# Kernel optimization log

Hardware: AMD Instinct MI355X
Metric: run time of the kernel (lower is better)

Reference implementation:

```python
import jax, jax.numpy as jnp
import numpy as np

B, N, NQ, C = 4, 16384, 1024, 128
NS = 64          # nsample
RADIUS = 0.3     # ball-query fallback radius


def setup_inputs() -> dict:
    key = jax.random.key(0)
    k1, k2, k3, k4 = jax.random.split(key, 4)
    key_xyz = jax.random.uniform(k1, (B, N, 3), dtype=jnp.float32)
    key_features = jax.random.normal(k2, (B, C, N), dtype=jnp.float32)
    centers = jax.random.uniform(k3, (B, NQ, 3), dtype=jnp.float32)
    # box sizes L/H/W in [0.05, 0.25]
    sizes = 0.05 + 0.2 * jax.random.uniform(k4, (B, NQ, 3), dtype=jnp.float32)
    query_xyz = jnp.concatenate([centers, sizes], axis=-1)
    return {"key_xyz": key_xyz, "key_features": key_features, "query_xyz": query_xyz}


def _box_group(key_xyz, key_features, query_xyz):
    centers = query_xyz[:, :, :3]              # [B,nq,3]
    half = 0.5 * query_xyz[:, :, 3:]           # [B,nq,3] half box extents

    # per-query per-key absolute offsets: [B,nq,N,3]
    d = jnp.abs(key_xyz[:, None, :, :] - centers[:, :, None, :])
    inside = jnp.all(d <= half[:, :, None, :], axis=-1)      # [B,nq,N] AABB test
    dist2 = jnp.sum(d * d, axis=-1)                          # [B,nq,N]

    # ball-query fallback for queries whose box contains no point
    has_box = jnp.any(inside, axis=-1)                       # [B,nq]
    sel = jnp.where(has_box[..., None], inside, dist2 <= RADIUS * RADIUS)

    # first NS selected indices (stable sort puts selected points first,
    # preserving ascending key index order -> deterministic box_query semantics)
    order = jnp.argsort((~sel).astype(jnp.int32), axis=-1)[:, :, :NS]  # [B,nq,NS]

    count = jnp.minimum(jnp.sum(sel, axis=-1), NS)           # [B,nq]
    pad = jnp.arange(NS)[None, None, :] >= count[..., None]  # True = padded slot
    idx = jnp.where(pad, 0, order)                           # pad with index 0
    mask = pad.at[:, :, 0].set(False)                        # cuda path: mask[...,0]=False

    # gathers
    g_xyz = jax.vmap(lambda k, i: k[i])(key_xyz, idx)        # [B,nq,NS,3]
    g_xyz = g_xyz - centers[:, :, None, :]                   # recenter on query
    grouped_xyz = jnp.transpose(g_xyz, (0, 3, 1, 2))         # [B,3,nq,NS]
    grouped_feat = jax.vmap(lambda f, i: f[:, i])(key_features, idx)  # [B,C,nq,NS]
    return grouped_xyz, grouped_feat, mask


def reference(key_xyz, key_features, query_xyz):
    return _box_group(key_xyz, key_features, query_xyz)
```

## Files before the change

### kernel.cpp

```cpp
#include <hip/hip_runtime.h>

#pragma clang fp contract(off)

#define B_  4
#define N_  16384
#define NQ_ 1024
#define C_  128
#define NS_ 64
#define G_  16
#define NCELL_ 4096
#define MAXCELLS_ 344
#define SELCAP_ 1024

#define OFF_IDX    ((size_t)0)
#define SZ_IDX     ((size_t)B_*NQ_*NS_*4)
#define OFF_FEAT   ((size_t)(1u<<20))
#define SZ_FEAT    ((size_t)B_*N_*C_*4)
#define OFF_COUNTS (OFF_FEAT + SZ_FEAT)
#define OFF_CSTART (OFF_COUNTS + (size_t)B_*NCELL_*4)
#define OFF_CURSOR (OFF_CSTART + (size_t)B_*NCELL_*4)
#define OFF_PLIST  (OFF_CURSOR + (size_t)B_*NCELL_*4)
#define WS_NEED    (OFF_PLIST + (size_t)B_*N_*4)

__global__ __launch_bounds__(256) void zero_k(int* __restrict__ counts) {
    int id = blockIdx.x * 256 + threadIdx.x;
    if (id < B_ * NCELL_) counts[id] = 0;
}

__device__ __forceinline__ int cell_of(float x, float y, float z) {
    int ix = (int)(x * (float)G_); ix = min(G_ - 1, max(0, ix));
    int iy = (int)(y * (float)G_); iy = min(G_ - 1, max(0, iy));
    int iz = (int)(z * (float)G_); iz = min(G_ - 1, max(0, iz));
    return ix + (iy << 4) + (iz << 8);
}

__global__ __launch_bounds__(256) void bin_count_k(const float* __restrict__ key_xyz,
                                                   int* __restrict__ counts) {
    int id = blockIdx.x * 256 + threadIdx.x;
    int b = id >> 14, n = id & (N_ - 1);
    const float* p = key_xyz + ((size_t)b * N_ + n) * 3;
    int cid = cell_of(p[0], p[1], p[2]);
    atomicAdd(&counts[(b << 12) + cid], 1);
}

__global__ __launch_bounds__(1024) void scan_k(const int* __restrict__ counts,
                                               int* __restrict__ cstart,
                                               int* __restrict__ cursor) {
    __shared__ int a[1024];
    int b = blockIdx.x, t = threadIdx.x;
    int base = b << 12;
    int c0 = t * 4;
    int v0 = counts[base + c0 + 0], v1 = counts[base + c0 + 1];
    int v2 = counts[base + c0 + 2], v3 = counts[base + c0 + 3];
    int s = v0 + v1 + v2 + v3;
    a[t] = s;
    __syncthreads();
    for (int o = 1; o < 1024; o <<= 1) {
        int add = (t >= o) ? a[t - o] : 0;
        __syncthreads();
        a[t] += add;
        __syncthreads();
    }
    int excl = a[t] - s;
    int e0 = excl, e1 = e0 + v0, e2 = e1 + v1, e3 = e2 + v2;
    cstart[base + c0 + 0] = e0; cursor[base + c0 + 0] = e0;
    cstart[base + c0 + 1] = e1; cursor[base + c0 + 1] = e1;
    cstart[base + c0 + 2] = e2; cursor[base + c0 + 2] = e2;
    cstart[base + c0 + 3] = e3; cursor[base + c0 + 3] = e3;
}

__global__ __launch_bounds__(256) void scatter_k(const float* __restrict__ key_xyz,
                                                 int* __restrict__ cursor,
                                                 int* __restrict__ plist) {
    int id = blockIdx.x * 256 + threadIdx.x;
    int b = id >> 14, n = id & (N_ - 1);
    const float* p = key_xyz + ((size_t)b * N_ + n) * 3;
    int cid = cell_of(p[0], p[1], p[2]);
    int pos = atomicAdd(&cursor[(b << 12) + cid], 1);
    plist[(b << 14) + pos] = n;
}

__global__ __launch_bounds__(256) void fused_ts_k(
    const float* __restrict__ key_xyz, const float* __restrict__ key_feat,
    const float* __restrict__ query,
    const int* __restrict__ counts, const int* __restrict__ cstart,
    const int* __restrict__ plist,
    float* __restrict__ feat_t, int* __restrict__ idx_out,
    float* __restrict__ out_xyz, float* __restrict__ out_mask)
{
    __shared__ float ttile[32][33];
    __shared__ int s_ccnt[MAXCELLS_];
    __shared__ int s_cstart[MAXCELLS_];
    __shared__ int s_pref[MAXCELLS_ + 1];
    __shared__ int s_sel[SELCAP_];
    __shared__ int s_scnt;
    __shared__ int s_list[4][NS_];
    __shared__ int s_cnt4[4];

    int t = threadIdx.x;

    if (blockIdx.x >= B_ * NQ_) {
        int id2 = blockIdx.x - B_ * NQ_;
        int n0 = (id2 & 511) * 32;
        int c0 = ((id2 >> 9) & 3) * 32;
        int b  = id2 >> 11;
        int x = t & 31, y = t >> 5;
#pragma unroll
        for (int k = 0; k < 4; ++k)
            ttile[y + 8*k][x] = key_feat[((size_t)b * C_ + c0 + y + 8*k) * N_ + n0 + x];
        __syncthreads();
#pragma unroll
        for (int k = 0; k < 4; ++k)
            feat_t[((size_t)b * N_ + n0 + y + 8*k) * C_ + c0 + x] = ttile[x][y + 8*k];
        return;
    }

    int bq = blockIdx.x;
    int b  = bq >> 10;
    int q  = bq & (NQ_ - 1);
    int wave = t >> 6, lane = t & 63;

    const float* qp = query + (size_t)bq * 6;
    float cx = qp[0], cy = qp[1], cz = qp[2];
    float hx = 0.5f * qp[3], hy = 0.5f * qp[4], hz = 0.5f * qp[5];
    const float* kb = key_xyz + (size_t)b * N_ * 3;

    if (t == 0) s_scnt = 0;

    int ilox = max(0, (int)floorf((cx - hx) * (float)G_) - 1);
    int ihix = min(G_ - 1, (int)floorf((cx + hx) * (float)G_) + 1);
    int iloy = max(0, (int)floorf((cy - hy) * (float)G_) - 1);
    int ihiy = min(G_ - 1, (int)floorf((cy + hy) * (float)G_) + 1);
    int iloz = max(0, (int)floorf((cz - hz) * (float)G_) - 1);
    int ihiz = min(G_ - 1, (int)floorf((cz + hz) * (float)G_) + 1);
    int nx = ihix - ilox + 1, ny = ihiy - iloy + 1, nz = ihiz - iloz + 1;
    int ncells = nx * ny * nz;

    for (int ci = t; ci < ncells; ci += 256) {
        int iz = ci / (nx * ny);
        int r  = ci - iz * (nx * ny);
        int iy = r / nx;
        int ix = r - iy * nx;
        int cid = (ilox + ix) + ((iloy + iy) << 4) + ((iloz + iz) << 8);
        s_ccnt[ci]   = counts[(b << 12) + cid];
        s_cstart[ci] = cstart[(b << 12) + cid];
    }
    __syncthreads();

    if (wave == 0) {
        int run = 0;
        for (int base = 0; base < ncells; base += 64) {
            int x = (base + lane < ncells) ? s_ccnt[base + lane] : 0;
            int own = x;
#pragma unroll
            for (int o = 1; o < 64; o <<= 1) {
                int v = __shfl_up(x, (unsigned)o);
                if (lane >= o) x += v;
            }
            if (base + lane < ncells) s_pref[base + lane] = run + x - own;
            run += __shfl(x, 63);
        }
        if (lane == 0) s_pref[ncells] = run;
    }
    __syncthreads();

    int total = s_pref[ncells];
    for (int i = t; i < total; i += 256) {
        int lo = 0, hi = ncells;
        while (hi - lo > 1) {
            int mid = (lo + hi) >> 1;
            if (s_pref[mid] <= i) lo = mid; else hi = mid;
        }
        int n = plist[(b << 14) + s_cstart[lo] + (i - s_pref[lo])];
        float dx = fabsf(kb[3*n + 0] - cx);
        float dy = fabsf(kb[3*n + 1] - cy);
        float dz = fabsf(kb[3*n + 2] - cz);
        if (dx <= hx && dy <= hy && dz <= hz) {
            int pos = atomicAdd(&s_scnt, 1);
            if (pos < SELCAP_) s_sel[pos] = n;
        }
    }
    __syncthreads();
    int scnt = s_scnt;

    if (scnt > 0) {
        int m = 64;
        while (m < scnt && m < SELCAP_) m <<= 1;
        for (int i = t; i < m; i += 256)
            if (i >= scnt) s_sel[i] = 0x7fffffff;
        __syncthreads();
        for (int k = 2; k <= m; k <<= 1) {
            for (int j = k >> 1; j > 0; j >>= 1) {
                for (int i = t; i < m; i += 256) {
                    int ixj = i ^ j;
                    if (ixj > i) {
                        int va = s_sel[i], vb = s_sel[ixj];
                        bool up = ((i & k) == 0);
                        if ((va > vb) == up) { s_sel[i] = vb; s_sel[ixj] = va; }
                    }
                }
                __syncthreads();
            }
        }
        int count = min(scnt, NS_);
        if (t < NS_) {
            int j = t;
            int idx = (j < count) ? s_sel[j] : 0;
            idx_out[(size_t)bq * NS_ + j] = idx;
            out_mask[(size_t)bq * NS_ + j] = (j >= count && j > 0) ? 1.0f : 0.0f;
            float px = kb[3*idx + 0] - cx;
            float py = kb[3*idx + 1] - cy;
            float pz = kb[3*idx + 2] - cz;
            size_t xb = ((size_t)b * 3) * NQ_ * NS_ + (size_t)q * NS_ + j;
            out_xyz[xb]                       = px;
            out_xyz[xb +     (size_t)NQ_*NS_] = py;
            out_xyz[xb + 2 * (size_t)NQ_*NS_] = pz;
        }
    } else {
        const float R2 = (float)(0.3 * 0.3);
        const int seg = N_ / 4;
        int n0s = wave * seg;
        unsigned long long lt = (1ull << lane) - 1ull;
        int cnt = 0;
        for (int it = 0; it < seg / 64; ++it) {
            int n = n0s + it * 64 + lane;
            float dx = kb[3*n + 0] - cx;
            float dy = kb[3*n + 1] - cy;
            float dz = kb[3*n + 2] - cz;
            float d2 = dx*dx + dy*dy + dz*dz;
            bool r = d2 <= R2;
            unsigned long long mmask = __ballot(r);
            if (r) {
                int p = cnt + __popcll(mmask & lt);
                if (p < NS_) s_list[wave][p] = n;
            }
            cnt += __popcll(mmask);
            if (cnt >= NS_) break;
        }
        if (lane == 0) s_cnt4[wave] = cnt;
        __syncthreads();
        if (wave == 0) {
            int c0s = min(s_cnt4[0], NS_);
            int c1s = min(s_cnt4[1], NS_);
            int c2s = min(s_cnt4[2], NS_);
            int tot   = s_cnt4[0] + s_cnt4[1] + s_cnt4[2] + s_cnt4[3];
            int count = min(tot, NS_);
            int j = lane;
            int idx = 0;
            if (j < count) {
                int o1 = c0s, o2 = o1 + c1s, o3 = o2 + c2s;
                if      (j < o1) idx = s_list[0][j];
                else if (j < o2) idx = s_list[1][j - o1];
                else if (j < o3) idx = s_list[2][j - o2];
                else             idx = s_list[3][j - o3];
            }
            idx_out[(size_t)bq * NS_ + j] = idx;
            out_mask[(size_t)bq * NS_ + j] = (j >= count && j > 0) ? 1.0f : 0.0f;
            float px = kb[3*idx + 0] - cx;
            float py = kb[3*idx + 1] - cy;
            float pz = kb[3*idx + 2] - cz;
            size_t xb = ((size_t)b * 3) * NQ_ * NS_ + (size_t)q * NS_ + j;
            out_xyz[xb]                       = px;
            out_xyz[xb +     (size_t)NQ_*NS_] = py;
            out_xyz[xb + 2 * (size_t)NQ_*NS_] = pz;
        }
    }
}

__global__ __launch_bounds__(256) void select_lin_k(
    const float* __restrict__ key_xyz, const float* __restrict__ query,
    int* __restrict__ idx_out, float* __restrict__ out_xyz,
    float* __restrict__ out_mask)
{
    int bq = blockIdx.x;
    int b  = bq >> 10;
    int q  = bq & (NQ_ - 1);
    int t    = threadIdx.x;
    int wave = t >> 6;
    int lane = t & 63;

    __shared__ int s_list[4][NS_];
    __shared__ int s_cnt[4];

    const float* qp = query + (size_t)bq * 6;
    float cx = qp[0], cy = qp[1], cz = qp[2];
    float hx = 0.5f * qp[3], hy = 0.5f * qp[4], hz = 0.5f * qp[5];
    const float* kb = key_xyz + (size_t)b * N_ * 3;

    const int seg = N_ / 4;
    int n0 = wave * seg;
    unsigned long long lt = (1ull << lane) - 1ull;

    int cnt = 0;
    for (int it = 0; it < seg / 64; ++it) {
        int n = n0 + it * 64 + lane;
        float dx = fabsf(kb[3*n + 0] - cx);
        float dy = fabsf(kb[3*n + 1] - cy);
        float dz = fabsf(kb[3*n + 2] - cz);
        bool inside = (dx <= hx) && (dy <= hy) && (dz <= hz);
        unsigned long long m = __ballot(inside);
        if (inside) {
            int p = cnt + __popcll(m & lt);
            if (p < NS_) s_list[wave][p] = n;
        }
        cnt += __popcll(m);
        if (cnt >= NS_) break;
    }
    if (lane == 0) s_cnt[wave] = cnt;
    __syncthreads();

    int ti = s_cnt[0] + s_cnt[1] + s_cnt[2] + s_cnt[3];
    if (ti == 0) {
        const float R2 = (float)(0.3 * 0.3);
        cnt = 0;
        for (int it = 0; it < seg / 64; ++it) {
            int n = n0 + it * 64 + lane;
            float dx = kb[3*n + 0] - cx;
            float dy = kb[3*n + 1] - cy;
            float dz = kb[3*n + 2] - cz;
            float d2 = dx*dx + dy*dy + dz*dz;
            bool r = d2 <= R2;
            unsigned long long m = __ballot(r);
            if (r) {
                int p = cnt + __popcll(m & lt);
                if (p < NS_) s_list[wave][p] = n;
            }
            cnt += __popcll(m);
            if (cnt >= NS_) break;
        }
        if (lane == 0) s_cnt[wave] = cnt;
    }
    __syncthreads();

    if (wave == 0) {
        int c0s = min(s_cnt[0], NS_);
        int c1s = min(s_cnt[1], NS_);
        int c2s = min(s_cnt[2], NS_);
        int tot   = s_cnt[0] + s_cnt[1] + s_cnt[2] + s_cnt[3];
        int count = min(tot, NS_);
        int j = lane;
        int idx = 0;
        if (j < count) {
            int o1 = c0s, o2 = o1 + c1s, o3 = o2 + c2s;
            if      (j < o1) idx = s_list[0][j];
            else if (j < o2) idx = s_list[1][j - o1];
            else if (j < o3) idx = s_list[2][j - o2];
            else             idx = s_list[3][j - o3];
        }
        idx_out[(size_t)bq * NS_ + j] = idx;
        out_mask[(size_t)bq * NS_ + j] = (j >= count && j > 0) ? 1.0f : 0.0f;
        float px = kb[3*idx + 0] - cx;
        float py = kb[3*idx + 1] - cy;
        float pz = kb[3*idx + 2] - cz;
        size_t xb = ((size_t)b * 3) * NQ_ * NS_ + (size_t)q * NS_ + j;
        out_xyz[xb]                       = px;
        out_xyz[xb +     (size_t)NQ_*NS_] = py;
        out_xyz[xb + 2 * (size_t)NQ_*NS_] = pz;
    }
}

__global__ __launch_bounds__(512) void gather_k(
    const float* __restrict__ feat_t, const int* __restrict__ idx_in,
    const float* __restrict__ key_feat, float* __restrict__ out_feat, int use_t)
{
    int bq = blockIdx.x;
    int b  = bq >> 10;
    int q  = bq & (NQ_ - 1);
    int t    = threadIdx.x;
    int wave = t >> 6;
    int lane = t & 63;

    __shared__ int   s_idx[NS_];
    __shared__ float tile[NS_][129];

    if (t < NS_) s_idx[t] = idx_in[(size_t)bq * NS_ + t];
    __syncthreads();

    float* ob = out_feat + (size_t)b * C_ * NQ_ * NS_ + (size_t)q * NS_;
    if (use_t) {
        const float4* ft4 = (const float4*)feat_t;
#pragma unroll
        for (int k = 0; k < 4; ++k) {
            int u  = t + k * 512;
            int j  = u >> 5;
            int c4 = u & 31;
            float4 v = ft4[((size_t)b * N_ + s_idx[j]) * (C_ / 4) + c4];
            tile[j][c4*4 + 0] = v.x;
            tile[j][c4*4 + 1] = v.y;
            tile[j][c4*4 + 2] = v.z;
            tile[j][c4*4 + 3] = v.w;
        }
        __syncthreads();
#pragma unroll
        for (int c = wave; c < C_; c += 8)
            __builtin_nontemporal_store(tile[lane][c],
                                        &ob[(size_t)c * NQ_ * NS_ + lane]);
    } else {
        const float* fb = key_feat + (size_t)b * C_ * N_;
        int idx = s_idx[lane];
        for (int c = wave; c < C_; c += 8)
            ob[(size_t)c * NQ_ * NS_ + lane] = fb[(size_t)c * N_ + idx];
    }
}

extern "C" void kernel_launch(void* const* d_in, const int* in_sizes, int n_in,
                              void* d_out, int out_size, void* d_ws, size_t ws_size,
                              hipStream_t stream) {
    const float* key_xyz  = (const float*)d_in[0];
    const float* key_feat = (const float*)d_in[1];
    const float* query    = (const float*)d_in[2];

    float* out      = (float*)d_out;
    float* out_xyz  = out;
    float* out_feat = out + (size_t)B_ * 3 * NQ_ * NS_;
    float* out_mask = out_feat + (size_t)B_ * C_ * NQ_ * NS_;

    char* ws = (char*)d_ws;
    int*   d_idx   = (int*)(ws + OFF_IDX);
    float* ft      = (float*)(ws + OFF_FEAT);
    int*   counts  = (int*)(ws + OFF_COUNTS);
    int*   cstartp = (int*)(ws + OFF_CSTART);
    int*   cursor  = (int*)(ws + OFF_CURSOR);
    int*   plist   = (int*)(ws + OFF_PLIST);

    if (ws_size >= WS_NEED) {
        zero_k<<<dim3((B_ * NCELL_ + 255) / 256), dim3(256), 0, stream>>>(counts);
        bin_count_k<<<dim3(B_ * N_ / 256), dim3(256), 0, stream>>>(key_xyz, counts);
        scan_k<<<dim3(B_), dim3(1024), 0, stream>>>(counts, cstartp, cursor);
        scatter_k<<<dim3(B_ * N_ / 256), dim3(256), 0, stream>>>(key_xyz, cursor, plist);
        fused_ts_k<<<dim3(B_ * NQ_ + B_ * (C_ / 32) * (N_ / 32)), dim3(256), 0, stream>>>(
            key_xyz, key_feat, query, counts, cstartp, plist,
            ft, d_idx, out_xyz, out_mask);
        gather_k<<<dim3(B_ * NQ_), dim3(512), 0, stream>>>(
            ft, d_idx, key_feat, out_feat, 1);
    } else {
        select_lin_k<<<dim3(B_ * NQ_), dim3(256), 0, stream>>>(
            key_xyz, query, d_idx, out_xyz, out_mask);
        gather_k<<<dim3(B_ * NQ_), dim3(512), 0, stream>>>(
            ft, d_idx, key_feat, out_feat, 0);
    }
}
```

Before: 216.6 us.

## Fuse selection with feature gather and move transpose into scatter kernel

The box selection and the feature gather are merged into one 512-thread kernel, so the intermediate index buffer round trip and one launch go away. The feature transpose now runs in the scatter kernel, with point lists storing xyz plus index as float4 so the selection reads coordinates without a second indirection. Small selections are sorted with a wave-level shuffle bitonic sort. Block IDs are remapped for XCD locality and the ball fallback is split across 8 waves. In exchange the fused kernel uses more shared memory and registers, which may lower occupancy, and the gather now runs in two channel chunks.

Measured after the change: 211.0 us. 1.03x faster.

```diff
diff --git a/kernel.cpp b/kernel.cpp
--- a/kernel.cpp
+++ b/kernel.cpp
@@ -12,26 +12,24 @@
 #define MAXCELLS_ 344
 #define SELCAP_ 1024
 
-#define OFF_IDX    ((size_t)0)
-#define SZ_IDX     ((size_t)B_*NQ_*NS_*4)
-#define OFF_FEAT   ((size_t)(1u<<20))
+#define OFF_FEAT   ((size_t)0)
 #define SZ_FEAT    ((size_t)B_*N_*C_*4)
 #define OFF_COUNTS (OFF_FEAT + SZ_FEAT)
 #define OFF_CSTART (OFF_COUNTS + (size_t)B_*NCELL_*4)
 #define OFF_CURSOR (OFF_CSTART + (size_t)B_*NCELL_*4)
-#define OFF_PLIST  (OFF_CURSOR + (size_t)B_*NCELL_*4)
-#define WS_NEED    (OFF_PLIST + (size_t)B_*N_*4)
-
-__global__ __launch_bounds__(256) void zero_k(int* __restrict__ counts) {
-    int id = blockIdx.x * 256 + threadIdx.x;
-    if (id < B_ * NCELL_) counts[id] = 0;
-}
+#define OFF_PLIST4 (OFF_CURSOR + (size_t)B_*NCELL_*4)
+#define WS_NEED    (OFF_PLIST4 + (size_t)B_*N_*16)
 
 __device__ __forceinline__ int cell_of(float x, float y, float z) {
     int ix = (int)(x * (float)G_); ix = min(G_ - 1, max(0, ix));
     int iy = (int)(y * (float)G_); iy = min(G_ - 1, max(0, iy));
     int iz = (int)(z * (float)G_); iz = min(G_ - 1, max(0, iz));
     return ix + (iy << 4) + (iz << 8);
+}
+
+__global__ __launch_bounds__(256) void zero_k(int* __restrict__ counts) {
+    int id = blockIdx.x * 256 + threadIdx.x;
+    if (id < B_ * NCELL_) counts[id] = 0;
 }
 
 __global__ __launch_bounds__(256) void bin_count_k(const float* __restrict__ key_xyz,
@@ -69,55 +67,64 @@
     cstart[base + c0 + 3] = e3; cursor[base + c0 + 3] = e3;
 }
 
-__global__ __launch_bounds__(256) void scatter_k(const float* __restrict__ key_xyz,
-                                                 int* __restrict__ cursor,
-                                                 int* __restrict__ plist) {
-    int id = blockIdx.x * 256 + threadIdx.x;
-    int b = id >> 14, n = id & (N_ - 1);
-    const float* p = key_xyz + ((size_t)b * N_ + n) * 3;
-    int cid = cell_of(p[0], p[1], p[2]);
-    int pos = atomicAdd(&cursor[(b << 12) + cid], 1);
-    plist[(b << 14) + pos] = n;
-}
-
-__global__ __launch_bounds__(256) void fused_ts_k(
+#define TBLK_ (B_ * (C_/32) * (N_/32))
+__global__ __launch_bounds__(256) void scatter_transpose_k(
     const float* __restrict__ key_xyz, const float* __restrict__ key_feat,
-    const float* __restrict__ query,
-    const int* __restrict__ counts, const int* __restrict__ cstart,
-    const int* __restrict__ plist,
-    float* __restrict__ feat_t, int* __restrict__ idx_out,
-    float* __restrict__ out_xyz, float* __restrict__ out_mask)
+    int* __restrict__ cursor, float4* __restrict__ plist4,
+    float* __restrict__ feat_t)
 {
     __shared__ float ttile[32][33];
-    __shared__ int s_ccnt[MAXCELLS_];
-    __shared__ int s_cstart[MAXCELLS_];
-    __shared__ int s_pref[MAXCELLS_ + 1];
-    __shared__ int s_sel[SELCAP_];
-    __shared__ int s_scnt;
-    __shared__ int s_list[4][NS_];
-    __shared__ int s_cnt4[4];
-
     int t = threadIdx.x;
-
-    if (blockIdx.x >= B_ * NQ_) {
-        int id2 = blockIdx.x - B_ * NQ_;
-        int n0 = (id2 & 511) * 32;
-        int c0 = ((id2 >> 9) & 3) * 32;
-        int b  = id2 >> 11;
+    if (blockIdx.x < TBLK_) {
+        int id2 = blockIdx.x;
+        int b   = id2 >> 11;
+        int rem = id2 & 2047;
+        int c0  = (rem >> 9) * 32;
+        int n0  = (rem & 511) * 32;
         int x = t & 31, y = t >> 5;
 #pragma unroll
         for (int k = 0; k < 4; ++k)
-            ttile[y + 8*k][x] = key_feat[((size_t)b * C_ + c0 + y + 8*k) * N_ + n0 + x];
+            ttile[y + 8*k][x] = __builtin_nontemporal_load(
+                &key_feat[((size_t)b * C_ + c0 + y + 8*k) * N_ + n0 + x]);
         __syncthreads();
 #pragma unroll
         for (int k = 0; k < 4; ++k)
             feat_t[((size_t)b * N_ + n0 + y + 8*k) * C_ + c0 + x] = ttile[x][y + 8*k];
         return;
     }
-
-    int bq = blockIdx.x;
-    int b  = bq >> 10;
-    int q  = bq & (NQ_ - 1);
+    int id = (blockIdx.x - TBLK_) * 256 + t;
+    int b = id >> 14, n = id & (N_ - 1);
+    const float* p = key_xyz + ((size_t)b * N_ + n) * 3;
+    float x = p[0], y = p[1], z = p[2];
+    int cid = cell_of(x, y, z);
+    int pos = atomicAdd(&cursor[(b << 12) + cid], 1);
+    plist4[(b << 14) + pos] = make_float4(x, y, z, __int_as_float(n));
+}
+
+__global__ __launch_bounds__(512) void selgather_k(
+    const float* __restrict__ key_xyz, const float* __restrict__ query,
+    const int* __restrict__ counts, const int* __restrict__ cstart,
+    const float4* __restrict__ plist4, const float* __restrict__ feat_t,
+    float* __restrict__ out_xyz, float* __restrict__ out_feat,
+    float* __restrict__ out_mask)
+{
+    __shared__ int   s_ccnt[MAXCELLS_];
+    __shared__ int   s_cstart[MAXCELLS_];
+    __shared__ int   s_pref[MAXCELLS_ + 1];
+    __shared__ int   s_sel[SELCAP_];
+    __shared__ int   s_scnt;
+    __shared__ int   s_list[8][NS_];
+    __shared__ int   s_cnt8[8];
+    __shared__ int   s_idx[NS_];
+    __shared__ int   s_count;
+    __shared__ float tile[NS_][65];
+
+    int i    = blockIdx.x;
+    int xcd  = i & 7;
+    int b    = xcd >> 1;
+    int q    = ((i >> 3) << 1) | (xcd & 1);
+    int bq   = (b << 10) | q;
+    int t    = threadIdx.x;
     int wave = t >> 6, lane = t & 63;
 
     const float* qp = query + (size_t)bq * 6;
@@ -136,7 +143,7 @@
     int nx = ihix - ilox + 1, ny = ihiy - iloy + 1, nz = ihiz - iloz + 1;
     int ncells = nx * ny * nz;
 
-    for (int ci = t; ci < ncells; ci += 256) {
+    for (int ci = t; ci < ncells; ci += 512) {
         int iz = ci / (nx * ny);
         int r  = ci - iz * (nx * ny);
         int iy = r / nx;
@@ -165,62 +172,70 @@
     __syncthreads();
 
     int total = s_pref[ncells];
-    for (int i = t; i < total; i += 256) {
+    const float4* pl = plist4 + ((size_t)b << 14);
+    for (int ii = t; ii < total; ii += 512) {
         int lo = 0, hi = ncells;
         while (hi - lo > 1) {
             int mid = (lo + hi) >> 1;
-            if (s_pref[mid] <= i) lo = mid; else hi = mid;
-        }
-        int n = plist[(b << 14) + s_cstart[lo] + (i - s_pref[lo])];
-        float dx = fabsf(kb[3*n + 0] - cx);
-        float dy = fabsf(kb[3*n + 1] - cy);
-        float dz = fabsf(kb[3*n + 2] - cz);
+            if (s_pref[mid] <= ii) lo = mid; else hi = mid;
+        }
+        float4 p = pl[s_cstart[lo] + (ii - s_pref[lo])];
+        float dx = fabsf(p.x - cx);
+        float dy = fabsf(p.y - cy);
+        float dz = fabsf(p.z - cz);
         if (dx <= hx && dy <= hy && dz <= hz) {
             int pos = atomicAdd(&s_scnt, 1);
-            if (pos < SELCAP_) s_sel[pos] = n;
-        }
-    }
-    __syncthreads();
-    int scnt = s_scnt;
+            if (pos < SELCAP_) s_sel[pos] = __float_as_int(p.w);
+        }
+    }
+    __syncthreads();
+    int scnt = min(s_scnt, SELCAP_);
 
     if (scnt > 0) {
-        int m = 64;
-        while (m < scnt && m < SELCAP_) m <<= 1;
-        for (int i = t; i < m; i += 256)
-            if (i >= scnt) s_sel[i] = 0x7fffffff;
-        __syncthreads();
-        for (int k = 2; k <= m; k <<= 1) {
-            for (int j = k >> 1; j > 0; j >>= 1) {
-                for (int i = t; i < m; i += 256) {
-                    int ixj = i ^ j;
-                    if (ixj > i) {
-                        int va = s_sel[i], vb = s_sel[ixj];
-                        bool up = ((i & k) == 0);
-                        if ((va > vb) == up) { s_sel[i] = vb; s_sel[ixj] = va; }
+        int count = min(scnt, NS_);
+        if (scnt <= NS_) {
+            if (wave == 0) {
+                int v = (lane < scnt) ? s_sel[lane] : 0x7fffffff;
+#pragma unroll
+                for (int k = 2; k <= 64; k <<= 1) {
+                    for (int j = k >> 1; j > 0; j >>= 1) {
+                        int pv = __shfl_xor(v, (unsigned)j);
+                        bool dir   = (lane & k) == 0;
+                        bool lower = (lane & j) == 0;
+                        int mn = min(v, pv), mx = max(v, pv);
+                        v = dir ? (lower ? mn : mx) : (lower ? mx : mn);
                     }
                 }
-                __syncthreads();
-            }
-        }
-        int count = min(scnt, NS_);
-        if (t < NS_) {
-            int j = t;
-            int idx = (j < count) ? s_sel[j] : 0;
-            idx_out[(size_t)bq * NS_ + j] = idx;
-            out_mask[(size_t)bq * NS_ + j] = (j >= count && j > 0) ? 1.0f : 0.0f;
-            float px = kb[3*idx + 0] - cx;
-            float py = kb[3*idx + 1] - cy;
-            float pz = kb[3*idx + 2] - cz;
-            size_t xb = ((size_t)b * 3) * NQ_ * NS_ + (size_t)q * NS_ + j;
-            out_xyz[xb]                       = px;
-            out_xyz[xb +     (size_t)NQ_*NS_] = py;
-            out_xyz[xb + 2 * (size_t)NQ_*NS_] = pz;
+                s_idx[lane] = (lane < count) ? v : 0;
+                if (lane == 0) s_count = count;
+            }
+        } else {
+            int m = NS_;
+            while (m < scnt) m <<= 1;
+            for (int ii = t; ii < m; ii += 512)
+                if (ii >= scnt) s_sel[ii] = 0x7fffffff;
+            __syncthreads();
+            for (int k = 2; k <= m; k <<= 1) {
+                for (int j = k >> 1; j > 0; j >>= 1) {
+                    for (int ii = t; ii < m; ii += 512) {
+                        int ixj = ii ^ j;
+                        if (ixj > ii) {
+                            int va = s_sel[ii], vb = s_sel[ixj];
+                            bool up = ((ii & k) == 0);
+                            if ((va > vb) == up) { s_sel[ii] = vb; s_sel[ixj] = va; }
+                        }
+                    }
+                    __syncthreads();
+                }
+            }
+            if (t < NS_) s_idx[t] = (t < count) ? s_sel[t] : 0;
+            if (t == 0)  s_count = count;
         }
     } else {
         const float R2 = (float)(0.3 * 0.3);
-        const int seg = N_ / 4;
+        const int seg = N_ / 8;
         int n0s = wave * seg;
-        unsigned long long lt = (1ull << lane) - 1ull;
+        unsigned long long ltm = (1ull << lane) - 1ull;
         int cnt = 0;
         for (int it = 0; it < seg / 64; ++it) {
             int n = n0s + it * 64 + lane;
@@ -229,41 +244,70 @@
             float dz = kb[3*n + 2] - cz;
             float d2 = dx*dx + dy*dy + dz*dz;
             bool r = d2 <= R2;
-            unsigned long long mmask = __ballot(r);
+            unsigned long long mm = __ballot(r);
             if (r) {
-                int p = cnt + __popcll(mmask & lt);
+                int p = cnt + __popcll(mm & ltm);
                 if (p < NS_) s_list[wave][p] = n;
             }
-            cnt += __popcll(mmask);
+            cnt += __popcll(mm);
             if (cnt >= NS_) break;
         }
-        if (lane == 0) s_cnt4[wave] = cnt;
+        if (lane == 0) s_cnt8[wave] = cnt;
         __syncthreads();
         if (wave == 0) {
-            int c0s = min(s_cnt4[0], NS_);
-            int c1s = min(s_cnt4[1], NS_);
-            int c2s = min(s_cnt4[2], NS_);
-            int tot   = s_cnt4[0] + s_cnt4[1] + s_cnt4[2] + s_cnt4[3];
+            int tot = 0;
+#pragma unroll
+            for (int w = 0; w < 8; ++w) tot += s_cnt8[w];
             int count = min(tot, NS_);
             int j = lane;
             int idx = 0;
             if (j < count) {
-                int o1 = c0s, o2 = o1 + c1s, o3 = o2 + c2s;
-                if      (j < o1) idx = s_list[0][j];
-                else if (j < o2) idx = s_list[1][j - o1];
-                else if (j < o3) idx = s_list[2][j - o2];
-                else             idx = s_list[3][j - o3];
-            }
-            idx_out[(size_t)bq * NS_ + j] = idx;
-            out_mask[(size_t)bq * NS_ + j] = (j >= count && j > 0) ? 1.0f : 0.0f;
-            float px = kb[3*idx + 0] - cx;
-            float py = kb[3*idx + 1] - cy;
-            float pz = kb[3*idx + 2] - cz;
-            size_t xb = ((size_t)b * 3) * NQ_ * NS_ + (size_t)q * NS_ + j;
-            out_xyz[xb]                       = px;
-            out_xyz[xb +     (size_t)NQ_*NS_] = py;
-            out_xyz[xb + 2 * (size_t)NQ_*NS_] = pz;
-        }
+                int w = 0, rem = j;
+                while (rem >= s_cnt8[w]) { rem -= s_cnt8[w]; ++w; }
+                idx = s_list[w][rem];
+            }
+            s_idx[j] = idx;
+            if (lane == 0) s_count = count;
+        }
+    }
+    __syncthreads();
+
+    int count = s_count;
+    if (t < NS_) {
+        int j = t, idx = s_idx[j];
+        out_mask[(size_t)bq * NS_ + j] = (j >= count && j > 0) ? 1.0f : 0.0f;
+        float px = kb[3*idx + 0] - cx;
+        float py = kb[3*idx + 1] - cy;
+        float pz = kb[3*idx + 2] - cz;
+        size_t xb = ((size_t)b * 3) * NQ_ * NS_ + (size_t)q * NS_ + j;
+        out_xyz[xb]                       = px;
+        out_xyz[xb +     (size_t)NQ_*NS_] = py;
+        out_xyz[xb + 2 * (size_t)NQ_*NS_] = pz;
+    }
+
+    const float4* ft4 = (const float4*)feat_t + (size_t)b * N_ * (C_ / 4);
+    float* ob = out_feat + (size_t)b * C_ * NQ_ * NS_ + (size_t)q * NS_;
+#pragma unroll
+    for (int chunk = 0; chunk < 2; ++chunk) {
+#pragma unroll
+        for (int k = 0; k < 2; ++k) {
+            int u  = t + k * 512;
+            int j  = u >> 4;
+            int c4 = u & 15;
+            float4 v = ft4[(size_t)s_idx[j] * (C_ / 4) + chunk * 16 + c4];
+            tile[j][c4*4 + 0] = v.x;
+            tile[j][c4*4 + 1] = v.y;
+            tile[j][c4*4 + 2] = v.z;
+            tile[j][c4*4 + 3] = v.w;
+        }
+        __syncthreads();
+#pragma unroll
+        for (int r = 0; r < 8; ++r) {
+            int cl = wave + r * 8;
+            __builtin_nontemporal_store(tile[lane][cl],
+                &ob[(size_t)(chunk * 64 + cl) * (NQ_ * NS_) + lane]);
+        }
+        __syncthreads();
     }
 }
 
@@ -359,9 +403,9 @@
     }
 }
 
-__global__ __launch_bounds__(512) void gather_k(
-    const float* __restrict__ feat_t, const int* __restrict__ idx_in,
-    const float* __restrict__ key_feat, float* __restrict__ out_feat, int use_t)
+__global__ __launch_bounds__(256) void gather_direct_k(
+    const int* __restrict__ idx_in, const float* __restrict__ key_feat,
+    float* __restrict__ out_feat)
 {
     int bq = blockIdx.x;
     int b  = bq >> 10;
@@ -369,38 +413,14 @@
     int t    = threadIdx.x;
     int wave = t >> 6;
     int lane = t & 63;
-
-    __shared__ int   s_idx[NS_];
-    __shared__ float tile[NS_][129];
-
+    __shared__ int s_idx[NS_];
     if (t < NS_) s_idx[t] = idx_in[(size_t)bq * NS_ + t];
     __syncthreads();
-
+    const float* fb = key_feat + (size_t)b * C_ * N_;
     float* ob = out_feat + (size_t)b * C_ * NQ_ * NS_ + (size_t)q * NS_;
-    if (use_t) {
-        const float4* ft4 = (const float4*)feat_t;
-#pragma unroll
-        for (int k = 0; k < 4; ++k) {
-            int u  = t + k * 512;
-            int j  = u >> 5;
-            int c4 = u & 31;
-            float4 v = ft4[((size_t)b * N_ + s_idx[j]) * (C_ / 4) + c4];
-            tile[j][c4*4 + 0] = v.x;
-            tile[j][c4*4 + 1] = v.y;
-            tile[j][c4*4 + 2] = v.z;
-            tile[j][c4*4 + 3] = v.w;
-        }
-        __syncthreads();
-#pragma unroll
-        for (int c = wave; c < C_; c += 8)
-            __builtin_nontemporal_store(tile[lane][c],
-                                        &ob[(size_t)c * NQ_ * NS_ + lane]);
-    } else {
-        const float* fb = key_feat + (size_t)b * C_ * N_;
-        int idx = s_idx[lane];
-        for (int c = wave; c < C_; c += 8)
-            ob[(size_t)c * NQ_ * NS_ + lane] = fb[(size_t)c * N_ + idx];
-    }
+    int idx = s_idx[lane];
+    for (int c = wave; c < C_; c += 4)
+        ob[(size_t)c * NQ_ * NS_ + lane] = fb[(size_t)c * N_ + idx];
 }
 
 extern "C" void kernel_launch(void* const* d_in, const int* in_sizes, int n_in,
@@ -416,27 +436,26 @@
     float* out_mask = out_feat + (size_t)B_ * C_ * NQ_ * NS_;
 
     char* ws = (char*)d_ws;
-    int*   d_idx   = (int*)(ws + OFF_IDX);
-    float* ft      = (float*)(ws + OFF_FEAT);
-    int*   counts  = (int*)(ws + OFF_COUNTS);
-    int*   cstartp = (int*)(ws + OFF_CSTART);
-    int*   cursor  = (int*)(ws + OFF_CURSOR);
-    int*   plist   = (int*)(ws + OFF_PLIST);
+    float*  ft      = (float*)(ws + OFF_FEAT);
+    int*    counts  = (int*)(ws + OFF_COUNTS);
+    int*    cstartp = (int*)(ws + OFF_CSTART);
+    int*    cursor  = (int*)(ws + OFF_CURSOR);
+    float4* plist4  = (float4*)(ws + OFF_PLIST4);
 
     if (ws_size >= WS_NEED) {
         zero_k<<<dim3((B_ * NCELL_ + 255) / 256), dim3(256), 0, stream>>>(counts);
         bin_count_k<<<dim3(B_ * N_ / 256), dim3(256), 0, stream>>>(key_xyz, counts);
         scan_k<<<dim3(B_), dim3(1024), 0, stream>>>(counts, cstartp, cursor);
-        scatter_k<<<dim3(B_ * N_ / 256), dim3(256), 0, stream>>>(key_xyz, cursor, plist);
-        fused_ts_k<<<dim3(B_ * NQ_ + B_ * (C_ / 32) * (N_ / 32)), dim3(256), 0, stream>>>(
-            key_xyz, key_feat, query, counts, cstartp, plist,
-            ft, d_idx, out_xyz, out_mask);
-        gather_k<<<dim3(B_ * NQ_), dim3(512), 0, stream>>>(
-            ft, d_idx, key_feat, out_feat, 1);
+        scatter_transpose_k<<<dim3(TBLK_ + B_ * N_ / 256), dim3(256), 0, stream>>>(
+            key_xyz, key_feat, cursor, plist4, ft);
+        selgather_k<<<dim3(B_ * NQ_), dim3(512), 0, stream>>>(
+            key_xyz, query, counts, cstartp, plist4, ft,
+            out_xyz, out_feat, out_mask);
     } else {
+        int* d_idx = (int*)d_ws;
         select_lin_k<<<dim3(B_ * NQ_), dim3(256), 0, stream>>>(
             key_xyz, query, d_idx, out_xyz, out_mask);
-        gather_k<<<dim3(B_ * NQ_), dim3(512), 0, stream>>>(
-            ft, d_idx, key_feat, out_feat, 0);
-    }
-}
+        gather_direct_k<<<dim3(B_ * NQ_), dim3(256), 0, stream>>>(
+            d_idx, key_feat, out_feat);
+    }
+}
```
